# Performance work log

Measured on AMD Instinct MI355X. Metric: run time of the kernel, lower is better.

Reference implementation:

```python
import jax, jax.numpy as jnp
import numpy as np

B = 131072
H = 192          # hidden_dim
NH = 4           # attention heads
HD = H // NH     # head dim = 48
MEM = 16         # resonance memory slots
GRID = 64        # 8x8 SOFM grid
DIMS = (("vib", 64), ("aco", 256), ("tmp", 128))


def setup_inputs() -> dict:
    key = jax.random.key(0)
    ks = iter(jax.random.split(key, 64))

    def nrm(shape, scale=0.02):
        return jax.random.normal(next(ks), shape, dtype=jnp.float32) * scale

    inp = {}
    inp["x_vib"] = jax.random.normal(next(ks), (B, 64), dtype=jnp.float32)
    inp["x_aco"] = jax.random.normal(next(ks), (B, 256), dtype=jnp.float32)
    inp["x_tmp"] = jax.random.normal(next(ks), (B, 128), dtype=jnp.float32)
    for m, d in DIMS:
        inp[f"enc_w_{m}"] = nrm((d, H))
        inp[f"enc_b_{m}"] = jnp.zeros((H,), jnp.float32)
        inp[f"enc_g_{m}"] = jnp.ones((H,), jnp.float32)
        inp[f"enc_bb_{m}"] = jnp.zeros((H,), jnp.float32)
    inp["fus_w"] = nrm((3 * H, H))
    inp["fus_b"] = jnp.zeros((H,), jnp.float32)
    inp["fus_g"] = jnp.ones((H,), jnp.float32)
    inp["fus_bb"] = jnp.zeros((H,), jnp.float32)
    inp["res_wq"] = nrm((3, H, H))
    inp["res_wk"] = nrm((3, H, H))
    inp["res_wv"] = nrm((3, H, H))
    inp["res_wo"] = nrm((3, H, H))
    inp["res_bq"] = jnp.zeros((3, H), jnp.float32)
    inp["res_bk"] = jnp.zeros((3, H), jnp.float32)
    inp["res_bv"] = jnp.zeros((3, H), jnp.float32)
    inp["res_bo"] = jnp.zeros((3, H), jnp.float32)
    inp["res_mem"] = nrm((3, MEM, H), 1.0)
    inp["grid"] = nrm((GRID, H), 1.0)
    inp["out_w"] = nrm((H, 6))
    inp["out_b"] = jnp.zeros((6,), jnp.float32)
    return inp


def _ln(x, g, b):
    m = x.mean(-1, keepdims=True)
    v = ((x - m) ** 2).mean(-1, keepdims=True)
    return (x - m) / jnp.sqrt(v + 1e-5) * g + b


def reference(x_vib, x_aco, x_tmp,
              enc_w_vib, enc_b_vib, enc_g_vib, enc_bb_vib,
              enc_w_aco, enc_b_aco, enc_g_aco, enc_bb_aco,
              enc_w_tmp, enc_b_tmp, enc_g_tmp, enc_bb_tmp,
              fus_w, fus_b, fus_g, fus_bb,
              res_wq, res_wk, res_wv, res_wo,
              res_bq, res_bk, res_bv, res_bo, res_mem,
              grid, out_w, out_b):
    # per-modality Linear + LayerNorm + GELU encoders
    feats = []
    for x, w, b, g, bb in ((x_vib, enc_w_vib, enc_b_vib, enc_g_vib, enc_bb_vib),
                           (x_aco, enc_w_aco, enc_b_aco, enc_g_aco, enc_bb_aco),
                           (x_tmp, enc_w_tmp, enc_b_tmp, enc_g_tmp, enc_bb_tmp)):
        feats.append(jax.nn.gelu(_ln(x @ w + b, g, bb), approximate=False))
    fused = jnp.concatenate(feats, axis=-1)                         # [B, 3H]
    fused = jax.nn.gelu(_ln(fused @ fus_w + fus_b, fus_g, fus_bb), approximate=False)

    # 3 adaptive resonance layers: cross-attention over a 16-slot memory bank
    scale = 1.0 / jnp.sqrt(jnp.float32(HD))
    for i in range(3):
        q = (fused @ res_wq[i] + res_bq[i]).reshape(-1, NH, HD)     # [B, h, d]
        k = (res_mem[i] @ res_wk[i] + res_bk[i]).reshape(MEM, NH, HD)
        v = (res_mem[i] @ res_wv[i] + res_bv[i]).reshape(MEM, NH, HD)
        scores = jnp.einsum("bhd,mhd->bhm", q, k) * scale           # [B, h, 16]
        attn = jax.nn.softmax(scores, axis=-1)
        o = jnp.einsum("bhm,mhd->bhd", attn, v).reshape(-1, H)
        fused = o @ res_wo[i] + res_bo[i]

    # SOFM: nearest-grid-vector lookup (squared dist has same argmin as cdist)
    d2 = (fused ** 2).sum(-1, keepdims=True) - 2.0 * (fused @ grid.T) + (grid ** 2).sum(-1)
    winners = jnp.argmin(d2, axis=1)                                # [B]
    fused = grid[winners]                                           # [B, H]

    pooled = fused.mean(axis=0)                                     # [H]
    out = pooled @ out_w + out_b                                    # [6]
    sig = jax.nn.sigmoid(out)
    # wear, remaining_life(relu), failure_prob, quality, confidence, anomaly
    return jnp.stack([sig[0], jax.nn.relu(out[1]), sig[2], sig[3], sig[4], sig[5]])
```

## Files before the change

kernel.cpp:

```cpp
#include <hip/hip_runtime.h>
#include <hip/hip_bf16.h>
#include <math.h>

typedef unsigned short ushort_t;
typedef __attribute__((ext_vector_type(8))) short short8;
typedef __attribute__((ext_vector_type(4))) float f32x4;

#define B_TOTAL 131072

#define OFF_VIB 0
#define OFF_ACO 12288
#define OFF_TMP 61440
#define OFF_FUS 86016
#define OFF_WK 196608
#define OFF_VPP 233472
#define OFF_GRID 270336
#define F32_BYTE_OFF 565248
#define F_KV 0
#define F_VV 9216
#define F_BS 18432
#define F_GGN 18624
#define F_CNT 18688

__device__ __forceinline__ ushort_t f2bu_prep(float f) {
  union { float f; unsigned u; } c; c.f = f;
  unsigned u = c.u;
  unsigned r = (u + 0x7fffu + ((u >> 16) & 1u)) >> 16;
  return (ushort_t)r;
}
__device__ __forceinline__ ushort_t f2bu(float f) {
  __hip_bfloat16 h = __float2bfloat16(f);
  return *(ushort_t*)&h;
}
__device__ __forceinline__ float fastrcp(float x) { return __builtin_amdgcn_rcpf(x); }
__device__ __forceinline__ float gelu_fast(float x) {
  float u = 0.7978845608f * x * (1.0f + 0.044715f * x * x);
  float E = exp2f(2.88539008f * u);
  float t = 1.0f - 2.0f * fastrcp(E + 1.0f);
  return 0.5f * x * (1.0f + t);
}
#define MFMA16(a, b, c) __builtin_amdgcn_mfma_f32_16x16x32_bf16(a, b, c, 0, 0, 0)

__device__ __forceinline__ void gload16(const void* g, void* l) {
  __builtin_amdgcn_global_load_lds((const __attribute__((address_space(1))) void*)g,
                                   (__attribute__((address_space(3))) void*)l, 16, 0, 0);
}

__global__ void prep_weights(const float* __restrict__ ev, const float* __restrict__ ea,
                             const float* __restrict__ et, const float* __restrict__ fw,
                             const float* __restrict__ gr, ushort_t* __restrict__ ws) {
  int tid = blockIdx.x * blockDim.x + threadIdx.x;
  int nth = gridDim.x * blockDim.x;
  for (int i = tid; i < 12288; i += nth) {
    int n = i >> 6, kin = i & 63;
    int k = 8 * ((kin >> 3) ^ (n & 7)) + (kin & 7);
    ws[OFF_VIB + i] = f2bu_prep(ev[k * 192 + n]);
  }
  for (int i = tid; i < 49152; i += nth) {
    int ck = i / 12288, rem = i % 12288, n = rem >> 6, kin = rem & 63;
    int k = ck * 64 + 8 * ((kin >> 3) ^ (n & 7)) + (kin & 7);
    ws[OFF_ACO + i] = f2bu_prep(ea[k * 192 + n]);
  }
  for (int i = tid; i < 24576; i += nth) {
    int ck = i / 12288, rem = i % 12288, n = rem >> 6, kin = rem & 63;
    int k = ck * 64 + 8 * ((kin >> 3) ^ (n & 7)) + (kin & 7);
    ws[OFF_TMP + i] = f2bu_prep(et[k * 192 + n]);
  }
  for (int i = tid; i < 110592; i += nth) {
    int ck = i / 12288, rem = i % 12288, n = rem >> 6, kin = rem & 63;
    int k = ck * 64 + 8 * ((kin >> 3) ^ (n & 7)) + (kin & 7);
    ws[OFF_FUS + i] = f2bu_prep(fw[k * 192 + n]);
  }
  for (int i = tid; i < 12288; i += nth) {
    int ck = i / 4096, rem = i % 4096, n = rem >> 6, kin = rem & 63;
    int k = ck * 64 + 8 * ((kin >> 3) ^ (n & 7)) + (kin & 7);
    ws[OFF_GRID + i] = f2bu_prep(gr[n * 192 + k]);
  }
}

__global__ void prep_kv1(const float* __restrict__ rwk, const float* __restrict__ rwv,
                         const float* __restrict__ rbk, const float* __restrict__ rbv,
                         const float* __restrict__ rmem, const float* __restrict__ gr,
                         float* __restrict__ wsf, unsigned* __restrict__ cnt) {
  int tid = blockIdx.x * blockDim.x + threadIdx.x;
  int nth = gridDim.x * blockDim.x;
  for (int idx = tid; idx < 18432; idx += nth) {
    int bank = idx / 9216, r = idx % 9216;
    int i = r / 3072, q = r % 3072, s = q / 192, d = q % 192;
    const float* w  = (bank ? rwv : rwk) + i * 36864;
    const float* bs = (bank ? rbv : rbk) + i * 192;
    const float* mm = rmem + i * 3072 + s * 192;
    float acc = bs[d];
    for (int kk = 0; kk < 192; ++kk) acc += mm[kk] * w[kk * 192 + d];
    wsf[bank * 9216 + (i * 16 + s) * 192 + d] = acc;
  }
  for (int g = tid; g < 64; g += nth) {
    const float* gp = gr + g * 192;
    float s = 0.f;
    for (int k = 0; k < 192; ++k) s += gp[k] * gp[k];
    wsf[F_GGN + g] = s;
    cnt[g] = 0u;
  }
}

__global__ void prep_kv2(const float* __restrict__ rwq, const float* __restrict__ rbq,
                         const float* __restrict__ rwo, const float* __restrict__ wsf,
                         ushort_t* __restrict__ ws, float* __restrict__ bS) {
  int tid = blockIdx.x * blockDim.x + threadIdx.x;
  int nth = gridDim.x * blockDim.x;
  const float scale = 0.144337567297406441f;
  const float* Kv = wsf + F_KV;
  const float* Vv = wsf + F_VV;
  for (int idx = tid; idx < 36864; idx += nth) {
    int i = idx / 12288, rem = idx % 12288;
    int ck = rem >> 12, r2 = rem & 4095, n = r2 >> 6, kin = r2 & 63;
    int k = ck * 64 + 8 * ((kin >> 3) ^ (n & 7)) + (kin & 7);
    int h = n >> 4, s = n & 15;
    const float* kvp = Kv + (i * 16 + s) * 192 + h * 48;
    const float* wqp = rwq + i * 36864 + k * 192 + h * 48;
    float acc = 0.f;
    for (int d = 0; d < 48; ++d) acc += wqp[d] * kvp[d];
    ws[OFF_WK + idx] = f2bu_prep(scale * acc);
  }
  for (int idx = tid; idx < 192; idx += nth) {
    int i = idx >> 6, n = idx & 63, h = n >> 4, s = n & 15;
    const float* kvp = Kv + (i * 16 + s) * 192 + h * 48;
    const float* bqp = rbq + i * 192 + h * 48;
    float acc = 0.f;
    for (int d = 0; d < 48; ++d) acc += bqp[d] * kvp[d];
    bS[idx] = scale * acc;
  }
  for (int idx = tid; idx < 36864; idx += nth) {
    int i = idx / 12288, rem = idx % 12288;
    int n = rem >> 6, kin = rem & 63;
    int k = 8 * ((kin >> 3) ^ (n & 7)) + (kin & 7);
    int h = k >> 4, s = k & 15;
    const float* vvp = Vv + (i * 16 + s) * 192 + h * 48;
    const float* wop = rwo + i * 36864 + (h * 48) * 192 + n;
    float acc = 0.f;
    for (int d = 0; d < 48; ++d) acc += vvp[d] * wop[d * 192];
    ws[OFF_VPP + idx] = f2bu_prep(acc);
  }
}

__device__ __forceinline__ void stage_to(ushort_t* dst, const ushort_t* src, int nseg,
                                         int wave, int lane) {
  for (int s = wave; s < nseg; s += 4)
    gload16(src + (s << 9) + lane * 8, dst + (s << 9));
}

__device__ __forceinline__ const ushort_t* chunk_ptr(const ushort_t* wsu, int g, int* nseg) {
  *nseg = 24;
  if (g < 1)            return wsu + OFF_VIB;
  g -= 1;  if (g < 3)   return wsu + OFF_FUS + g * 12288;
  g -= 3;  if (g < 4)   return wsu + OFF_ACO + g * 12288;
  g -= 4;  if (g < 3)   return wsu + OFF_FUS + 36864 + g * 12288;
  g -= 3;  if (g < 2)   return wsu + OFF_TMP + g * 12288;
  g -= 2;  if (g < 3)   return wsu + OFF_FUS + 73728 + g * 12288;
  g -= 3;  if (g < 12)  { int l = g >> 2, r2 = g & 3;
    if (r2 < 3) { *nseg = 8; return wsu + OFF_WK + l * 12288 + r2 * 4096; }
    return wsu + OFF_VPP + l * 12288; }
  g -= 12; if (g < 3)   { *nseg = 8; return wsu + OFF_GRID + g * 4096; }
  *nseg = 0; return wsu;
}

__device__ __forceinline__ void phase_begin(const ushort_t* wsu, ushort_t (*Wb)[12288],
                                            int gph, int wave, int lane) {
  __syncthreads();
  int nseg; const ushort_t* ns = chunk_ptr(wsu, gph + 1, &nseg);
  if (nseg) stage_to(&Wb[(gph + 1) & 1][0], ns, nseg, wave, lane);
}

__device__ __forceinline__ short8 cvt8(float4 a, float4 b) {
  short8 v;
  v[0] = (short)f2bu(a.x); v[1] = (short)f2bu(a.y); v[2] = (short)f2bu(a.z); v[3] = (short)f2bu(a.w);
  v[4] = (short)f2bu(b.x); v[5] = (short)f2bu(b.y); v[6] = (short)f2bu(b.z); v[7] = (short)f2bu(b.w);
  return v;
}

template<int NPH>
__device__ __forceinline__ void enc_gemm(const float* __restrict__ x, int row0,
    const ushort_t* wsu, ushort_t (*Wb)[12288], int* gph, f32x4* accE,
    int m, int gq, int wave, int lane) {
  const int KF = NPH * 64;
  const float* p0 = x + (size_t)row0 * KF + gq * 8;
  float4 ca0 = *(const float4*)(p0);
  float4 ca1 = *(const float4*)(p0 + 4);
#pragma unroll
  for (int ph = 0; ph < NPH; ++ph) {
    phase_begin(wsu, Wb, *gph, wave, lane);
    const ushort_t* Wc = &Wb[*gph & 1][0];
#pragma unroll
    for (int ks = 0; ks < 2; ++ks) {
      int sl = ks * 4 + gq;
      short8 a = cvt8(ca0, ca1);
      int nk = ph * 64 + ks * 32 + 32;
      if (nk < KF) {
        ca0 = *(const float4*)(p0 + nk);
        ca1 = *(const float4*)(p0 + nk + 4);
      }
#pragma unroll
      for (int t = 0; t < 12; ++t) {
        int n = t * 16 + m;
        short8 b = *(const short8*)(Wc + n * 64 + ((sl ^ (n & 7)) << 3));
        accE[t] = MFMA16(b, a, accE[t]);
      }
    }
    ++*gph;
  }
}

__device__ __forceinline__ void lds_gemm(const ushort_t* Ab, const ushort_t* wsu,
    ushort_t (*Wb)[12288], int* gph, f32x4* acc, int wc0, int m, int gq,
    int wave, int lane) {
#pragma unroll
  for (int ph = 0; ph < 3; ++ph) {
    phase_begin(wsu, Wb, *gph, wave, lane);
    const ushort_t* Wc = &Wb[*gph & 1][0];
#pragma unroll
    for (int ks = 0; ks < 2; ++ks) {
      int sl = ks * 4 + gq;
      short8 b0, b1, b2;
      {
        int n0 = wc0 + m, n1 = wc0 + 16 + m, n2 = wc0 + 32 + m;
        b0 = *(const short8*)(Wc + n0 * 64 + ((sl ^ (n0 & 7)) << 3));
        b1 = *(const short8*)(Wc + n1 * 64 + ((sl ^ (n1 & 7)) << 3));
        b2 = *(const short8*)(Wc + n2 * 64 + ((sl ^ (n2 & 7)) << 3));
      }
#pragma unroll
      for (int mt = 0; mt < 4; ++mt) {
        int r = mt * 16 + m;
        short8 a = *(const short8*)(Ab + r * 192 + ((ph * 8 + (sl ^ (r & 7))) << 3));
        acc[mt * 3 + 0] = MFMA16(b0, a, acc[mt * 3 + 0]);
        acc[mt * 3 + 1] = MFMA16(b1, a, acc[mt * 3 + 1]);
        acc[mt * 3 + 2] = MFMA16(b2, a, acc[mt * 3 + 2]);
      }
    }
    ++*gph;
  }
}

__device__ __forceinline__ void ln_gelu_enc(f32x4* acc, const float* __restrict__ bias,
    const float* __restrict__ gam, const float* __restrict__ bet,
    ushort_t* __restrict__ Ab, int rloc, int gq) {
  float s = 0.f, q = 0.f;
#pragma unroll
  for (int t = 0; t < 12; ++t) {
    float4 bv = *(const float4*)(bias + t * 16 + gq * 4);
#pragma unroll
    for (int j = 0; j < 4; ++j) {
      float v = acc[t][j] + ((const float*)&bv)[j];
      acc[t][j] = v; s += v; q += v * v;
    }
  }
  s += __shfl_xor(s, 16, 64); q += __shfl_xor(q, 16, 64);
  s += __shfl_xor(s, 32, 64); q += __shfl_xor(q, 32, 64);
  float mean = s * (1.0f / 192.0f);
  float var = q * (1.0f / 192.0f) - mean * mean;
  float rstd = rsqrtf(var + 1e-5f);
#pragma unroll
  for (int t = 0; t < 12; ++t) {
    int colb = t * 16 + gq * 4;
    float4 ga = *(const float4*)(gam + colb);
    float4 be = *(const float4*)(bet + colb);
    ushort_t o[4];
#pragma unroll
    for (int j = 0; j < 4; ++j) {
      float y = (acc[t][j] - mean) * rstd * ((const float*)&ga)[j] + ((const float*)&be)[j];
      o[j] = f2bu(gelu_fast(y));
    }
    int off = rloc * 192 + (((colb >> 3) ^ (rloc & 7)) << 3) + (colb & 7);
    *(uint2*)(Ab + off) = *(uint2*)o;
  }
}

__device__ __forceinline__ void ln_gelu_fus(f32x4* acc, const float* __restrict__ bias,
    const float* __restrict__ gam, const float* __restrict__ bet,
    ushort_t* __restrict__ Ab, float2 (*scr)[4], int wave, int wc0, int m, int gq) {
  float4 bv[3];
#pragma unroll
  for (int t = 0; t < 3; ++t) bv[t] = *(const float4*)(bias + wc0 + t * 16 + gq * 4);
#pragma unroll
  for (int mt = 0; mt < 4; ++mt) {
    float s = 0.f, q = 0.f;
#pragma unroll
    for (int t = 0; t < 3; ++t)
#pragma unroll
      for (int j = 0; j < 4; ++j) {
        float v = acc[mt * 3 + t][j] + ((const float*)&bv[t])[j];
        acc[mt * 3 + t][j] = v; s += v; q += v * v;
      }
    s += __shfl_xor(s, 16, 64); q += __shfl_xor(q, 16, 64);
    s += __shfl_xor(s, 32, 64); q += __shfl_xor(q, 32, 64);
    if (gq == 0) scr[mt * 16 + m][wave] = (float2){s, q};
  }
  __syncthreads();
#pragma unroll
  for (int mt = 0; mt < 4; ++mt) {
    int row = mt * 16 + m;
    float s = 0.f, q = 0.f;
#pragma unroll
    for (int w = 0; w < 4; ++w) { float2 p = scr[row][w]; s += p.x; q += p.y; }
    float mean = s * (1.0f / 192.0f);
    float var = q * (1.0f / 192.0f) - mean * mean;
    float rstd = rsqrtf(var + 1e-5f);
#pragma unroll
    for (int t = 0; t < 3; ++t) {
      int colb = wc0 + t * 16 + gq * 4;
      float4 ga = *(const float4*)(gam + colb);
      float4 be = *(const float4*)(bet + colb);
      ushort_t o[4];
#pragma unroll
      for (int j = 0; j < 4; ++j) {
        float y = (acc[mt * 3 + t][j] - mean) * rstd * ((const float*)&ga)[j] + ((const float*)&be)[j];
        o[j] = f2bu(gelu_fast(y));
      }
      int off = row * 192 + (((colb >> 3) ^ (row & 7)) << 3) + (colb & 7);
      *(uint2*)(Ab + off) = *(uint2*)o;
    }
  }
}

__device__ __forceinline__ void bias_store_cs(f32x4* acc, const float* __restrict__ bias,
    ushort_t* __restrict__ Ab, int wc0, int m, int gq) {
  float4 bv[3];
#pragma unroll
  for (int t = 0; t < 3; ++t) bv[t] = *(const float4*)(bias + wc0 + t * 16 + gq * 4);
#pragma unroll
  for (int mt = 0; mt < 4; ++mt) {
    int row = mt * 16 + m;
#pragma unroll
    for (int t = 0; t < 3; ++t) {
      int colb = wc0 + t * 16 + gq * 4;
      ushort_t o[4];
#pragma unroll
      for (int j = 0; j < 4; ++j)
        o[j] = f2bu(acc[mt * 3 + t][j] + ((const float*)&bv[t])[j]);
      int off = row * 192 + (((colb >> 3) ^ (row & 7)) << 3) + (colb & 7);
      *(uint2*)(Ab + off) = *(uint2*)o;
    }
  }
}

__global__ __launch_bounds__(256) __attribute__((amdgpu_waves_per_eu(2))) void arn_main(
    const float* __restrict__ xv, const float* __restrict__ xa, const float* __restrict__ xt,
    const ushort_t* __restrict__ wsu, const float* __restrict__ bS,
    const float* __restrict__ ggn, unsigned* __restrict__ counts,
    const float* __restrict__ ebv, const float* __restrict__ egv, const float* __restrict__ ebbv,
    const float* __restrict__ eba, const float* __restrict__ ega, const float* __restrict__ ebba,
    const float* __restrict__ ebt, const float* __restrict__ egt, const float* __restrict__ ebbt,
    const float* __restrict__ fb, const float* __restrict__ fg, const float* __restrict__ fbb,
    const float* __restrict__ rbo) {
  __shared__ __align__(16) ushort_t Abuf[64 * 192 + 64];
  __shared__ __align__(16) ushort_t Wbuf[2][12288];
  __shared__ float2 lnscr[64][4];
  __shared__ __align__(16) float c_l[64];
  __shared__ unsigned hist[64];

  const int tid = threadIdx.x, lane = tid & 63, wave = tid >> 6;
  const int m = lane & 15, gq = lane >> 4;
  const int wc0 = wave * 48;
  const int w16 = wave * 16;
  const int growbase = blockIdx.x * 64;

  if (tid < 64) { hist[tid] = 0u; c_l[tid] = 0.5f * ggn[tid]; Abuf[12288 + tid] = 0; }

  int gph = 0;
  { int nseg; const ushort_t* s0 = chunk_ptr(wsu, 0, &nseg); stage_to(&Wbuf[0][0], s0, nseg, wave, lane); }

  const int row0 = growbase + w16 + m;
  const int rloc = w16 + m;
  f32x4 accF[12];
#pragma unroll
  for (int t = 0; t < 12; ++t) accF[t] = (f32x4){0.f, 0.f, 0.f, 0.f};

  {
    f32x4 accE[12];
#pragma unroll
    for (int t = 0; t < 12; ++t) accE[t] = (f32x4){0.f, 0.f, 0.f, 0.f};
    enc_gemm<1>(xv, row0, wsu, Wbuf, &gph, accE, m, gq, wave, lane);
    ln_gelu_enc(accE, ebv, egv, ebbv, Abuf, rloc, gq);
  }
  lds_gemm(Abuf, wsu, Wbuf, &gph, accF, wc0, m, gq, wave, lane);

  {
    f32x4 accE[12];
#pragma unroll
    for (int t = 0; t < 12; ++t) accE[t] = (f32x4){0.f, 0.f, 0.f, 0.f};
    enc_gemm<4>(xa, row0, wsu, Wbuf, &gph, accE, m, gq, wave, lane);
    ln_gelu_enc(accE, eba, ega, ebba, Abuf, rloc, gq);
  }
  lds_gemm(Abuf, wsu, Wbuf, &gph, accF, wc0, m, gq, wave, lane);

  {
    f32x4 accE[12];
#pragma unroll
    for (int t = 0; t < 12; ++t) accE[t] = (f32x4){0.f, 0.f, 0.f, 0.f};
    enc_gemm<2>(xt, row0, wsu, Wbuf, &gph, accE, m, gq, wave, lane);
    ln_gelu_enc(accE, ebt, egt, ebbt, Abuf, rloc, gq);
  }
  lds_gemm(Abuf, wsu, Wbuf, &gph, accF, wc0, m, gq, wave, lane);
  ln_gelu_fus(accF, fb, fg, fbb, Abuf, lnscr, wave, wc0, m, gq);

  for (int i = 0; i < 3; ++i) {
    f32x4 accS[4];
#pragma unroll
    for (int t = 0; t < 4; ++t) accS[t] = (f32x4){0.f, 0.f, 0.f, 0.f};
#pragma unroll
    for (int ph = 0; ph < 3; ++ph) {
      phase_begin(wsu, Wbuf, gph, wave, lane);
      const ushort_t* Wc = &Wbuf[gph & 1][0];
      int n = w16 + m;
#pragma unroll
      for (int ks = 0; ks < 2; ++ks) {
        int sl = ks * 4 + gq;
        short8 b = *(const short8*)(Wc + n * 64 + ((sl ^ (n & 7)) << 3));
#pragma unroll
        for (int mt = 0; mt < 4; ++mt) {
          int r = mt * 16 + m;
          short8 a = *(const short8*)(Abuf + r * 192 + ((ph * 8 + (sl ^ (r & 7))) << 3));
          accS[mt] = MFMA16(b, a, accS[mt]);
        }
      }
      ++gph;
    }
    {
      ushort_t* Pb = &Wbuf[0][0] + 8192;
      float4 bS4 = *(const float4*)(bS + i * 64 + w16 + gq * 4);
      const int gnum = (w16 + gq * 4) >> 3;
#pragma unroll
      for (int mt = 0; mt < 4; ++mt) {
        float e[4]; float mx = -3.0e38f;
#pragma unroll
        for (int j = 0; j < 4; ++j) { e[j] = accS[mt][j] + ((const float*)&bS4)[j]; mx = fmaxf(mx, e[j]); }
        mx = fmaxf(mx, __shfl_xor(mx, 16, 64));
        mx = fmaxf(mx, __shfl_xor(mx, 32, 64));
        float sm = 0.f;
#pragma unroll
        for (int j = 0; j < 4; ++j) { e[j] = exp2f((e[j] - mx) * 1.44269504f); sm += e[j]; }
        sm += __shfl_xor(sm, 16, 64);
        sm += __shfl_xor(sm, 32, 64);
        float inv = fastrcp(sm);
        ushort_t p4[4];
#pragma unroll
        for (int j = 0; j < 4; ++j) p4[j] = f2bu(e[j] * inv);
        int r = mt * 16 + m;
        *(uint2*)(Pb + r * 64 + ((gnum ^ (r & 7)) << 3) + (gq & 1) * 4) = *(uint2*)p4;
      }
    }
    {
      f32x4 accO[12];
#pragma unroll
      for (int t = 0; t < 12; ++t) accO[t] = (f32x4){0.f, 0.f, 0.f, 0.f};
      phase_begin(wsu, Wbuf, gph, wave, lane);
      const ushort_t* Wc = &Wbuf[gph & 1][0];
      const ushort_t* Pb = &Wbuf[0][0] + 8192;
#pragma unroll
      for (int ks = 0; ks < 2; ++ks) {
        int sl = ks * 4 + gq;
        short8 b0, b1, b2;
        {
          int n0 = wc0 + m, n1 = wc0 + 16 + m, n2 = wc0 + 32 + m;
          b0 = *(const short8*)(Wc + n0 * 64 + ((sl ^ (n0 & 7)) << 3));
          b1 = *(const short8*)(Wc + n1 * 64 + ((sl ^ (n1 & 7)) << 3));
          b2 = *(const short8*)(Wc + n2 * 64 + ((sl ^ (n2 & 7)) << 3));
        }
#pragma unroll
        for (int mt = 0; mt < 4; ++mt) {
          int r = mt * 16 + m;
          short8 a = *(const short8*)(Pb + r * 64 + ((sl ^ (r & 7)) << 3));
          accO[mt * 3 + 0] = MFMA16(b0, a, accO[mt * 3 + 0]);
          accO[mt * 3 + 1] = MFMA16(b1, a, accO[mt * 3 + 1]);
          accO[mt * 3 + 2] = MFMA16(b2, a, accO[mt * 3 + 2]);
        }
      }
      ++gph;
      bias_store_cs(accO, rbo + i * 192, Abuf, wc0, m, gq);
    }
  }

  {
    f32x4 accS[4];
#pragma unroll
    for (int t = 0; t < 4; ++t) accS[t] = (f32x4){0.f, 0.f, 0.f, 0.f};
#pragma unroll
    for (int ph = 0; ph < 3; ++ph) {
      phase_begin(wsu, Wbuf, gph, wave, lane);
      const ushort_t* Wc = &Wbuf[gph & 1][0];
      int r = w16 + m;
#pragma unroll
      for (int ks = 0; ks < 2; ++ks) {
        int sl = ks * 4 + gq;
        short8 a = *(const short8*)(Abuf + r * 192 + ((ph * 8 + (sl ^ (r & 7))) << 3));
#pragma unroll
        for (int nt = 0; nt < 4; ++nt) {
          int n = nt * 16 + m;
          short8 b = *(const short8*)(Wc + n * 64 + ((sl ^ (n & 7)) << 3));
          accS[nt] = MFMA16(b, a, accS[nt]);
        }
      }
      ++gph;
    }
    float bv = -3.0e38f; int bi = 64;
#pragma unroll
    for (int nt = 0; nt < 4; ++nt) {
      int gb = nt * 16 + gq * 4;
      float4 cl = *(const float4*)(c_l + gb);
#pragma unroll
      for (int j = 0; j < 4; ++j) {
        float v = accS[nt][j] - ((const float*)&cl)[j];
        int g = gb + j;
        bool take = (v > bv);
        bv = take ? v : bv; bi = take ? g : bi;
      }
    }
#pragma unroll
    for (int off = 16; off < 64; off <<= 1) {
      float ov = __shfl_xor(bv, off, 64);
      int oi = __shfl_xor(bi, off, 64);
      bool take = (ov > bv) || (ov == bv && oi < bi);
      bv = take ? ov : bv; bi = take ? oi : bi;
    }
    if (gq == 0) atomicAdd(&hist[bi], 1u);
  }
  __syncthreads();
  if (tid < 64 && hist[tid]) atomicAdd(&counts[tid], hist[tid]);
}

__global__ void arn_finish(const unsigned* __restrict__ counts, const float* __restrict__ gr,
                           const float* __restrict__ ow, const float* __restrict__ ob,
                           float* __restrict__ out) {
  __shared__ float pooled[192];
  __shared__ float cf[64];
  int t = threadIdx.x;
  if (t < 64) cf[t] = (float)counts[t];
  __syncthreads();
  float s = 0.f;
  for (int g = 0; g < 64; ++g) s += cf[g] * gr[g * 192 + t];
  pooled[t] = s * (1.0f / (float)B_TOTAL);
  __syncthreads();
  if (t < 6) {
    float o = ob[t];
    for (int j = 0; j < 192; ++j) o += pooled[j] * ow[j * 6 + t];
    out[t] = (t == 1) ? fmaxf(o, 0.f) : 1.f / (1.f + expf(-o));
  }
}

extern "C" void kernel_launch(void* const* d_in, const int* in_sizes, int n_in,
                              void* d_out, int out_size, void* d_ws, size_t ws_size,
                              hipStream_t stream) {
  (void)in_sizes; (void)n_in; (void)out_size; (void)ws_size;
  const float* xv   = (const float*)d_in[0];
  const float* xa   = (const float*)d_in[1];
  const float* xt   = (const float*)d_in[2];
  const float* ewv  = (const float*)d_in[3];
  const float* ebv  = (const float*)d_in[4];
  const float* egv  = (const float*)d_in[5];
  const float* ebbv = (const float*)d_in[6];
  const float* ewa  = (const float*)d_in[7];
  const float* eba  = (const float*)d_in[8];
  const float* ega  = (const float*)d_in[9];
  const float* ebba = (const float*)d_in[10];
  const float* ewt  = (const float*)d_in[11];
  const float* ebt  = (const float*)d_in[12];
  const float* egt  = (const float*)d_in[13];
  const float* ebbt = (const float*)d_in[14];
  const float* fw   = (const float*)d_in[15];
  const float* fb   = (const float*)d_in[16];
  const float* fg   = (const float*)d_in[17];
  const float* fbb  = (const float*)d_in[18];
  const float* rwq  = (const float*)d_in[19];
  const float* rwk  = (const float*)d_in[20];
  const float* rwv  = (const float*)d_in[21];
  const float* rwo  = (const float*)d_in[22];
  const float* rbq  = (const float*)d_in[23];
  const float* rbk  = (const float*)d_in[24];
  const float* rbv  = (const float*)d_in[25];
  const float* rbo  = (const float*)d_in[26];
  const float* rmem = (const float*)d_in[27];
  const float* grid = (const float*)d_in[28];
  const float* ow   = (const float*)d_in[29];
  const float* ob   = (const float*)d_in[30];

  ushort_t* wsu = (ushort_t*)d_ws;
  float* wsf = (float*)((char*)d_ws + F32_BYTE_OFF);
  float* bS  = wsf + F_BS;
  float* ggn = wsf + F_GGN;
  unsigned* cnt = (unsigned*)(wsf + F_CNT);

  prep_weights<<<dim3(256), dim3(256), 0, stream>>>(ewv, ewa, ewt, fw, grid, wsu);
  prep_kv1<<<dim3(80), dim3(256), 0, stream>>>(rwk, rwv, rbk, rbv, rmem, grid, wsf, cnt);
  prep_kv2<<<dim3(80), dim3(256), 0, stream>>>(rwq, rbq, rwo, wsf, wsu, bS);
  arn_main<<<dim3(2048), dim3(256), 0, stream>>>(xv, xa, xt, wsu, bS, ggn, cnt,
      ebv, egv, ebbv, eba, ega, ebba, ebt, egt, ebbt, fb, fg, fbb, rbo);
  arn_finish<<<dim3(1), dim3(192), 0, stream>>>(cnt, grid, ow, ob, (float*)d_out);
}
```

Before: 227.7 us.

## Fold attention output projections into next-layer score and grid matrices

Each layer's attention-output product (P·V·Wo) is pre-multiplied with the next layer's query/key projection, and the last one with the SOFM grid, in a new prep kernel. The main kernel therefore chains 64-wide softmax probability tiles through small 64x64 GEMMs and never materialises the 192-wide fused activation between attention layers. Biases and grid norms are folded into per-column constants. This removes the three 192-wide output GEMMs and most of the weight staging, but adds an extra bf16 rounding of the composed matrices and one more prep launch.

```diff
diff --git a/kernel.cpp b/kernel.cpp
--- a/kernel.cpp
+++ b/kernel.cpp
@@ -13,14 +13,16 @@
 #define OFF_TMP 61440
 #define OFF_FUS 86016
 #define OFF_WK 196608
-#define OFF_VPP 233472
-#define OFF_GRID 270336
-#define F32_BYTE_OFF 565248
+#define OFF_M 208896
+#define F32_BYTE_OFF 442368
 #define F_KV 0
 #define F_VV 9216
-#define F_BS 18432
-#define F_GGN 18624
-#define F_CNT 18688
+#define F_VPP 18432
+#define F_WKF 55296
+#define F_BSF 92160
+#define F_BATTN 92352
+#define F_BG 92544
+#define F_CNT 92608
 
 __device__ __forceinline__ ushort_t f2bu_prep(float f) {
   union { float f; unsigned u; } c; c.f = f;
@@ -48,7 +50,7 @@
 
 __global__ void prep_weights(const float* __restrict__ ev, const float* __restrict__ ea,
                              const float* __restrict__ et, const float* __restrict__ fw,
-                             const float* __restrict__ gr, ushort_t* __restrict__ ws) {
+                             ushort_t* __restrict__ ws) {
   int tid = blockIdx.x * blockDim.x + threadIdx.x;
   int nth = gridDim.x * blockDim.x;
   for (int i = tid; i < 12288; i += nth) {
@@ -71,17 +73,12 @@
     int k = ck * 64 + 8 * ((kin >> 3) ^ (n & 7)) + (kin & 7);
     ws[OFF_FUS + i] = f2bu_prep(fw[k * 192 + n]);
   }
-  for (int i = tid; i < 12288; i += nth) {
-    int ck = i / 4096, rem = i % 4096, n = rem >> 6, kin = rem & 63;
-    int k = ck * 64 + 8 * ((kin >> 3) ^ (n & 7)) + (kin & 7);
-    ws[OFF_GRID + i] = f2bu_prep(gr[n * 192 + k]);
-  }
 }
 
 __global__ void prep_kv1(const float* __restrict__ rwk, const float* __restrict__ rwv,
                          const float* __restrict__ rbk, const float* __restrict__ rbv,
-                         const float* __restrict__ rmem, const float* __restrict__ gr,
-                         float* __restrict__ wsf, unsigned* __restrict__ cnt) {
+                         const float* __restrict__ rmem, float* __restrict__ wsf,
+                         unsigned* __restrict__ cnt) {
   int tid = blockIdx.x * blockDim.x + threadIdx.x;
   int nth = gridDim.x * blockDim.x;
   for (int idx = tid; idx < 18432; idx += nth) {
@@ -94,33 +91,47 @@
     for (int kk = 0; kk < 192; ++kk) acc += mm[kk] * w[kk * 192 + d];
     wsf[bank * 9216 + (i * 16 + s) * 192 + d] = acc;
   }
-  for (int g = tid; g < 64; g += nth) {
-    const float* gp = gr + g * 192;
-    float s = 0.f;
-    for (int k = 0; k < 192; ++k) s += gp[k] * gp[k];
-    wsf[F_GGN + g] = s;
-    cnt[g] = 0u;
-  }
+  for (int g = tid; g < 64; g += nth) cnt[g] = 0u;
 }
 
 __global__ void prep_kv2(const float* __restrict__ rwq, const float* __restrict__ rbq,
-                         const float* __restrict__ rwo, const float* __restrict__ wsf,
-                         ushort_t* __restrict__ ws, float* __restrict__ bS) {
+                         const float* __restrict__ rwo, float* __restrict__ wsf,
+                         ushort_t* __restrict__ ws) {
   int tid = blockIdx.x * blockDim.x + threadIdx.x;
   int nth = gridDim.x * blockDim.x;
   const float scale = 0.144337567297406441f;
   const float* Kv = wsf + F_KV;
   const float* Vv = wsf + F_VV;
+  float* WKf = wsf + F_WKF;
+  float* Vpp = wsf + F_VPP;
+  float* bSf = wsf + F_BSF;
   for (int idx = tid; idx < 36864; idx += nth) {
-    int i = idx / 12288, rem = idx % 12288;
-    int ck = rem >> 12, r2 = rem & 4095, n = r2 >> 6, kin = r2 & 63;
-    int k = ck * 64 + 8 * ((kin >> 3) ^ (n & 7)) + (kin & 7);
+    int i = idx / 12288, rem = idx % 12288, n = rem / 192, k = rem % 192;
     int h = n >> 4, s = n & 15;
     const float* kvp = Kv + (i * 16 + s) * 192 + h * 48;
     const float* wqp = rwq + i * 36864 + k * 192 + h * 48;
     float acc = 0.f;
     for (int d = 0; d < 48; ++d) acc += wqp[d] * kvp[d];
+    WKf[idx] = scale * acc;
+  }
+  for (int idx = tid; idx < 12288; idx += nth) {
+    int ck = idx >> 12, r2 = idx & 4095, n = r2 >> 6, kin = r2 & 63;
+    int k = ck * 64 + 8 * ((kin >> 3) ^ (n & 7)) + (kin & 7);
+    int h = n >> 4, s = n & 15;
+    const float* kvp = Kv + s * 192 + h * 48;
+    const float* wqp = rwq + k * 192 + h * 48;
+    float acc = 0.f;
+    for (int d = 0; d < 48; ++d) acc += wqp[d] * kvp[d];
     ws[OFF_WK + idx] = f2bu_prep(scale * acc);
+  }
+  for (int idx = tid; idx < 36864; idx += nth) {
+    int i = idx / 12288, rem = idx % 12288, n = rem / 192, dcol = rem % 192;
+    int h = n >> 4, s = n & 15;
+    const float* vvp = Vv + (i * 16 + s) * 192 + h * 48;
+    const float* wop = rwo + i * 36864 + (h * 48) * 192 + dcol;
+    float acc = 0.f;
+    for (int d = 0; d < 48; ++d) acc += vvp[d] * wop[d * 192];
+    Vpp[idx] = acc;
   }
   for (int idx = tid; idx < 192; idx += nth) {
     int i = idx >> 6, n = idx & 63, h = n >> 4, s = n & 15;
@@ -128,18 +139,51 @@
     const float* bqp = rbq + i * 192 + h * 48;
     float acc = 0.f;
     for (int d = 0; d < 48; ++d) acc += bqp[d] * kvp[d];
-    bS[idx] = scale * acc;
-  }
-  for (int idx = tid; idx < 36864; idx += nth) {
-    int i = idx / 12288, rem = idx % 12288;
-    int n = rem >> 6, kin = rem & 63;
+    bSf[idx] = scale * acc;
+  }
+}
+
+__global__ void prep_kv3(const float* __restrict__ rbo, const float* __restrict__ gr,
+                         float* __restrict__ wsf, ushort_t* __restrict__ ws) {
+  int tid = blockIdx.x * blockDim.x + threadIdx.x;
+  int nth = gridDim.x * blockDim.x;
+  const float* Vpp = wsf + F_VPP;
+  const float* WKf = wsf + F_WKF;
+  const float* bSf = wsf + F_BSF;
+  for (int idx = tid; idx < 8192; idx += nth) {
+    int l = idx >> 12, rem = idx & 4095, n = rem >> 6, kin = rem & 63;
     int k = 8 * ((kin >> 3) ^ (n & 7)) + (kin & 7);
-    int h = k >> 4, s = k & 15;
-    const float* vvp = Vv + (i * 16 + s) * 192 + h * 48;
-    const float* wop = rwo + i * 36864 + (h * 48) * 192 + n;
+    const float* vp = Vpp + l * 12288 + k * 192;
+    const float* wp = WKf + (l + 1) * 12288 + n * 192;
     float acc = 0.f;
-    for (int d = 0; d < 48; ++d) acc += vvp[d] * wop[d * 192];
-    ws[OFF_VPP + idx] = f2bu_prep(acc);
+    for (int t = 0; t < 192; ++t) acc += vp[t] * wp[t];
+    ws[OFF_M + l * 4096 + n * 64 + kin] = f2bu_prep(acc);
+  }
+  for (int idx = tid; idx < 4096; idx += nth) {
+    int n = idx >> 6, kin = idx & 63;
+    int k = 8 * ((kin >> 3) ^ (n & 7)) + (kin & 7);
+    const float* vp = Vpp + 2 * 12288 + k * 192;
+    const float* gp = gr + n * 192;
+    float acc = 0.f;
+    for (int t = 0; t < 192; ++t) acc += vp[t] * gp[t];
+    ws[OFF_M + 8192 + n * 64 + kin] = f2bu_prep(acc);
+  }
+  for (int idx = tid; idx < 192; idx += nth) {
+    int l = idx >> 6, n = idx & 63;
+    float acc = bSf[l * 64 + n];
+    if (l > 0) {
+      const float* wp = WKf + l * 12288 + n * 192;
+      const float* bo = rbo + (l - 1) * 192;
+      for (int t = 0; t < 192; ++t) acc += bo[t] * wp[t];
+    }
+    wsf[F_BATTN + idx] = acc;
+  }
+  for (int g = tid; g < 64; g += nth) {
+    const float* gp = gr + g * 192;
+    const float* bo = rbo + 2 * 192;
+    float a = 0.f, s = 0.f;
+    for (int t = 0; t < 192; ++t) { a += bo[t] * gp[t]; s += gp[t] * gp[t]; }
+    wsf[F_BG + g] = a - 0.5f * s;
   }
 }
 
@@ -157,10 +201,8 @@
   g -= 4;  if (g < 3)   return wsu + OFF_FUS + 36864 + g * 12288;
   g -= 3;  if (g < 2)   return wsu + OFF_TMP + g * 12288;
   g -= 2;  if (g < 3)   return wsu + OFF_FUS + 73728 + g * 12288;
-  g -= 3;  if (g < 12)  { int l = g >> 2, r2 = g & 3;
-    if (r2 < 3) { *nseg = 8; return wsu + OFF_WK + l * 12288 + r2 * 4096; }
-    return wsu + OFF_VPP + l * 12288; }
-  g -= 12; if (g < 3)   { *nseg = 8; return wsu + OFF_GRID + g * 4096; }
+  g -= 3;  if (g < 3)   { *nseg = 8; return wsu + OFF_WK + g * 4096; }
+  g -= 3;  if (g < 3)   { *nseg = 8; return wsu + OFF_M + g * 4096; }
   *nseg = 0; return wsu;
 }
 
@@ -321,40 +363,42 @@
   }
 }
 
-__device__ __forceinline__ void bias_store_cs(f32x4* acc, const float* __restrict__ bias,
-    ushort_t* __restrict__ Ab, int wc0, int m, int gq) {
-  float4 bv[3];
-#pragma unroll
-  for (int t = 0; t < 3; ++t) bv[t] = *(const float4*)(bias + wc0 + t * 16 + gq * 4);
+__device__ __forceinline__ void softmax_to_P(f32x4* accS, const float* __restrict__ bptr,
+    ushort_t* __restrict__ Pb, int w16, int m, int gq) {
+  float4 b4 = *(const float4*)(bptr + w16 + gq * 4);
+  const int gnum = (w16 + gq * 4) >> 3;
 #pragma unroll
   for (int mt = 0; mt < 4; ++mt) {
-    int row = mt * 16 + m;
-#pragma unroll
-    for (int t = 0; t < 3; ++t) {
-      int colb = wc0 + t * 16 + gq * 4;
-      ushort_t o[4];
-#pragma unroll
-      for (int j = 0; j < 4; ++j)
-        o[j] = f2bu(acc[mt * 3 + t][j] + ((const float*)&bv[t])[j]);
-      int off = row * 192 + (((colb >> 3) ^ (row & 7)) << 3) + (colb & 7);
-      *(uint2*)(Ab + off) = *(uint2*)o;
-    }
+    float e[4]; float mx = -3.0e38f;
+#pragma unroll
+    for (int j = 0; j < 4; ++j) { e[j] = accS[mt][j] + ((const float*)&b4)[j]; mx = fmaxf(mx, e[j]); }
+    mx = fmaxf(mx, __shfl_xor(mx, 16, 64));
+    mx = fmaxf(mx, __shfl_xor(mx, 32, 64));
+    float sm = 0.f;
+#pragma unroll
+    for (int j = 0; j < 4; ++j) { e[j] = exp2f((e[j] - mx) * 1.44269504f); sm += e[j]; }
+    sm += __shfl_xor(sm, 16, 64);
+    sm += __shfl_xor(sm, 32, 64);
+    float inv = fastrcp(sm);
+    ushort_t p4[4];
+#pragma unroll
+    for (int j = 0; j < 4; ++j) p4[j] = f2bu(e[j] * inv);
+    int r = mt * 16 + m;
+    *(uint2*)(Pb + r * 64 + ((gnum ^ (r & 7)) << 3) + (gq & 1) * 4) = *(uint2*)p4;
   }
 }
 
 __global__ __launch_bounds__(256) __attribute__((amdgpu_waves_per_eu(2))) void arn_main(
     const float* __restrict__ xv, const float* __restrict__ xa, const float* __restrict__ xt,
-    const ushort_t* __restrict__ wsu, const float* __restrict__ bS,
-    const float* __restrict__ ggn, unsigned* __restrict__ counts,
+    const ushort_t* __restrict__ wsu, const float* __restrict__ battn,
+    const float* __restrict__ bG, unsigned* __restrict__ counts,
     const float* __restrict__ ebv, const float* __restrict__ egv, const float* __restrict__ ebbv,
     const float* __restrict__ eba, const float* __restrict__ ega, const float* __restrict__ ebba,
     const float* __restrict__ ebt, const float* __restrict__ egt, const float* __restrict__ ebbt,
-    const float* __restrict__ fb, const float* __restrict__ fg, const float* __restrict__ fbb,
-    const float* __restrict__ rbo) {
+    const float* __restrict__ fb, const float* __restrict__ fg, const float* __restrict__ fbb) {
   __shared__ __align__(16) ushort_t Abuf[64 * 192 + 64];
   __shared__ __align__(16) ushort_t Wbuf[2][12288];
   __shared__ float2 lnscr[64][4];
-  __shared__ __align__(16) float c_l[64];
   __shared__ unsigned hist[64];
 
   const int tid = threadIdx.x, lane = tid & 63, wave = tid >> 6;
@@ -363,7 +407,7 @@
   const int w16 = wave * 16;
   const int growbase = blockIdx.x * 64;
 
-  if (tid < 64) { hist[tid] = 0u; c_l[tid] = 0.5f * ggn[tid]; Abuf[12288 + tid] = 0; }
+  if (tid < 64) { hist[tid] = 0u; Abuf[12288 + tid] = 0; }
 
   int gph = 0;
   { int nseg; const ushort_t* s0 = chunk_ptr(wsu, 0, &nseg); stage_to(&Wbuf[0][0], s0, nseg, wave, lane); }
@@ -402,7 +446,7 @@
   lds_gemm(Abuf, wsu, Wbuf, &gph, accF, wc0, m, gq, wave, lane);
   ln_gelu_fus(accF, fb, fg, fbb, Abuf, lnscr, wave, wc0, m, gq);
 
-  for (int i = 0; i < 3; ++i) {
+  {
     f32x4 accS[4];
 #pragma unroll
     for (int t = 0; t < 4; ++t) accS[t] = (f32x4){0.f, 0.f, 0.f, 0.f};
@@ -424,104 +468,73 @@
       }
       ++gph;
     }
-    {
-      ushort_t* Pb = &Wbuf[0][0] + 8192;
-      float4 bS4 = *(const float4*)(bS + i * 64 + w16 + gq * 4);
-      const int gnum = (w16 + gq * 4) >> 3;
-#pragma unroll
-      for (int mt = 0; mt < 4; ++mt) {
-        float e[4]; float mx = -3.0e38f;
-#pragma unroll
-        for (int j = 0; j < 4; ++j) { e[j] = accS[mt][j] + ((const float*)&bS4)[j]; mx = fmaxf(mx, e[j]); }
-        mx = fmaxf(mx, __shfl_xor(mx, 16, 64));
-        mx = fmaxf(mx, __shfl_xor(mx, 32, 64));
-        float sm = 0.f;
-#pragma unroll
-        for (int j = 0; j < 4; ++j) { e[j] = exp2f((e[j] - mx) * 1.44269504f); sm += e[j]; }
-        sm += __shfl_xor(sm, 16, 64);
-        sm += __shfl_xor(sm, 32, 64);
-        float inv = fastrcp(sm);
-        ushort_t p4[4];
-#pragma unroll
-        for (int j = 0; j < 4; ++j) p4[j] = f2bu(e[j] * inv);
-        int r = mt * 16 + m;
-        *(uint2*)(Pb + r * 64 + ((gnum ^ (r & 7)) << 3) + (gq & 1) * 4) = *(uint2*)p4;
-      }
-    }
-    {
-      f32x4 accO[12];
-#pragma unroll
-      for (int t = 0; t < 12; ++t) accO[t] = (f32x4){0.f, 0.f, 0.f, 0.f};
+    softmax_to_P(accS, battn, &Wbuf[(gph - 1) & 1][8192], w16, m, gq);
+
+#pragma unroll
+    for (int l = 1; l <= 2; ++l) {
+      const ushort_t* Pprev = &Wbuf[(gph & 1) ^ 1][8192];
+#pragma unroll
+      for (int t = 0; t < 4; ++t) accS[t] = (f32x4){0.f, 0.f, 0.f, 0.f};
       phase_begin(wsu, Wbuf, gph, wave, lane);
       const ushort_t* Wc = &Wbuf[gph & 1][0];
-      const ushort_t* Pb = &Wbuf[0][0] + 8192;
+      int n = w16 + m;
 #pragma unroll
       for (int ks = 0; ks < 2; ++ks) {
         int sl = ks * 4 + gq;
-        short8 b0, b1, b2;
-        {
-          int n0 = wc0 + m, n1 = wc0 + 16 + m, n2 = wc0 + 32 + m;
-          b0 = *(const short8*)(Wc + n0 * 64 + ((sl ^ (n0 & 7)) << 3));
-          b1 = *(const short8*)(Wc + n1 * 64 + ((sl ^ (n1 & 7)) << 3));
-          b2 = *(const short8*)(Wc + n2 * 64 + ((sl ^ (n2 & 7)) << 3));
-        }
+        short8 b = *(const short8*)(Wc + n * 64 + ((sl ^ (n & 7)) << 3));
 #pragma unroll
         for (int mt = 0; mt < 4; ++mt) {
           int r = mt * 16 + m;
-          short8 a = *(const short8*)(Pb + r * 64 + ((sl ^ (r & 7)) << 3));
-          accO[mt * 3 + 0] = MFMA16(b0, a, accO[mt * 3 + 0]);
-          accO[mt * 3 + 1] = MFMA16(b1, a, accO[mt * 3 + 1]);
-          accO[mt * 3 + 2] = MFMA16(b2, a, accO[mt * 3 + 2]);
+          short8 a = *(const short8*)(Pprev + r * 64 + ((sl ^ (r & 7)) << 3));
+          accS[mt] = MFMA16(b, a, accS[mt]);
         }
       }
       ++gph;
-      bias_store_cs(accO, rbo + i * 192, Abuf, wc0, m, gq);
-    }
-  }
-
-  {
-    f32x4 accS[4];
-#pragma unroll
-    for (int t = 0; t < 4; ++t) accS[t] = (f32x4){0.f, 0.f, 0.f, 0.f};
-#pragma unroll
-    for (int ph = 0; ph < 3; ++ph) {
+      softmax_to_P(accS, battn + l * 64, &Wbuf[(gph - 1) & 1][8192], w16, m, gq);
+    }
+
+    {
+      const ushort_t* P3 = &Wbuf[(gph & 1) ^ 1][8192];
+      f32x4 accG[4];
+#pragma unroll
+      for (int t = 0; t < 4; ++t) accG[t] = (f32x4){0.f, 0.f, 0.f, 0.f};
       phase_begin(wsu, Wbuf, gph, wave, lane);
       const ushort_t* Wc = &Wbuf[gph & 1][0];
       int r = w16 + m;
 #pragma unroll
       for (int ks = 0; ks < 2; ++ks) {
         int sl = ks * 4 + gq;
-        short8 a = *(const short8*)(Abuf + r * 192 + ((ph * 8 + (sl ^ (r & 7))) << 3));
+        short8 a = *(const short8*)(P3 + r * 64 + ((sl ^ (r & 7)) << 3));
 #pragma unroll
         for (int nt = 0; nt < 4; ++nt) {
           int n = nt * 16 + m;
           short8 b = *(const short8*)(Wc + n * 64 + ((sl ^ (n & 7)) << 3));
-          accS[nt] = MFMA16(b, a, accS[nt]);
+          accG[nt] = MFMA16(b, a, accG[nt]);
         }
       }
       ++gph;
-    }
-    float bv = -3.0e38f; int bi = 64;
-#pragma unroll
-    for (int nt = 0; nt < 4; ++nt) {
-      int gb = nt * 16 + gq * 4;
-      float4 cl = *(const float4*)(c_l + gb);
-#pragma unroll
-      for (int j = 0; j < 4; ++j) {
-        float v = accS[nt][j] - ((const float*)&cl)[j];
-        int g = gb + j;
-        bool take = (v > bv);
-        bv = take ? v : bv; bi = take ? g : bi;
-      }
-    }
-#pragma unroll
-    for (int off = 16; off < 64; off <<= 1) {
-      float ov = __shfl_xor(bv, off, 64);
-      int oi = __shfl_xor(bi, off, 64);
-      bool take = (ov > bv) || (ov == bv && oi < bi);
-      bv = take ? ov : bv; bi = take ? oi : bi;
-    }
-    if (gq == 0) atomicAdd(&hist[bi], 1u);
+      float bv = -3.0e38f; int bi = 64;
+#pragma unroll
+      for (int nt = 0; nt < 4; ++nt) {
+        int gb = nt * 16 + gq * 4;
+        float4 g4 = *(const float4*)(bG + gb);
+#pragma unroll
+        for (int j = 0; j < 4; ++j) {
+          float v = accG[nt][j] + ((const float*)&g4)[j];
+          int g = gb + j;
+          bool take = (v > bv);
+          bv = take ? v : bv; bi = take ? g : bi;
+        }
+      }
+#pragma unroll
+      for (int off = 16; off < 64; off <<= 1) {
+        float ov = __shfl_xor(bv, off, 64);
+        int oi = __shfl_xor(bi, off, 64);
+        bool take = (ov > bv) || (ov == bv && oi < bi);
+        bv = take ? ov : bv; bi = take ? oi : bi;
+      }
+      if (gq == 0) atomicAdd(&hist[bi], 1u);
+    }
   }
   __syncthreads();
   if (tid < 64 && hist[tid]) atomicAdd(&counts[tid], hist[tid]);
@@ -584,14 +597,15 @@
 
   ushort_t* wsu = (ushort_t*)d_ws;
   float* wsf = (float*)((char*)d_ws + F32_BYTE_OFF);
-  float* bS  = wsf + F_BS;
-  float* ggn = wsf + F_GGN;
+  float* battn = wsf + F_BATTN;
+  float* bG    = wsf + F_BG;
   unsigned* cnt = (unsigned*)(wsf + F_CNT);
 
-  prep_weights<<<dim3(256), dim3(256), 0, stream>>>(ewv, ewa, ewt, fw, grid, wsu);
-  prep_kv1<<<dim3(80), dim3(256), 0, stream>>>(rwk, rwv, rbk, rbv, rmem, grid, wsf, cnt);
-  prep_kv2<<<dim3(80), dim3(256), 0, stream>>>(rwq, rbq, rwo, wsf, wsu, bS);
-  arn_main<<<dim3(2048), dim3(256), 0, stream>>>(xv, xa, xt, wsu, bS, ggn, cnt,
-      ebv, egv, ebbv, eba, ega, ebba, ebt, egt, ebbt, fb, fg, fbb, rbo);
+  prep_weights<<<dim3(256), dim3(256), 0, stream>>>(ewv, ewa, ewt, fw, wsu);
+  prep_kv1<<<dim3(80), dim3(256), 0, stream>>>(rwk, rwv, rbk, rbv, rmem, wsf, cnt);
+  prep_kv2<<<dim3(120), dim3(256), 0, stream>>>(rwq, rbq, rwo, wsf, wsu);
+  prep_kv3<<<dim3(64), dim3(256), 0, stream>>>(rbo, grid, wsf, wsu);
+  arn_main<<<dim3(2048), dim3(256), 0, stream>>>(xv, xa, xt, wsu, battn, bG, cnt,
+      ebv, egv, ebbv, eba, ega, ebba, ebt, egt, ebbt, fb, fg, fbb);
   arn_finish<<<dim3(1), dim3(192), 0, stream>>>(cnt, grid, ow, ob, (float*)d_out);
 }
```

After: 218.8 us. -3.9%, faster.
